# Kernel optimization log

Measured on AMD Instinct MI355X. Metric: run time of the kernel, lower is better.

## Reference

```python
import jax, jax.numpy as jnp
import numpy as np

N_NODES = 100000
N_EDGES = 1280000
IN_CH = 500
TEXT_DIM = 384
HIDDEN = 64
OUT_CH = 7


def _gcn_conv(h, w, b, src, dst, n):
    """PyG GCNConv: linear -> add self-loops -> sym-normalized sum aggregation -> bias.
    Self-loops handled analytically (adds deg+1 and a dinv[i]^2-scaled self message)
    to avoid materializing extra edges."""
    h = h @ w  # [n, out]
    ones = jnp.ones((src.shape[0],), h.dtype)
    deg = jax.ops.segment_sum(ones, dst, num_segments=n) + 1.0  # in-degree incl. self-loop
    dinv = deg ** -0.5
    coef = dinv[src] * dinv[dst]  # [E]
    msg = h[src] * coef[:, None]  # gather + normalize
    agg = jax.ops.segment_sum(msg, dst, num_segments=n)  # scatter-add
    agg = agg + h * (dinv * dinv)[:, None]  # self-loop contribution
    return agg + b


def setup_inputs() -> dict:
    key = jax.random.key(0)
    ks = jax.random.split(key, 12)
    f32 = jnp.float32
    x = jax.random.normal(ks[0], (N_NODES, IN_CH), f32)
    text_x = jax.random.normal(ks[1], (N_NODES, TEXT_DIM), f32)
    edge_index = jax.random.randint(ks[2], (2, N_EDGES), 0, N_NODES, dtype=jnp.int64)
    def lin(k, fan_in, fan_out):
        s = 1.0 / np.sqrt(fan_in)
        return jax.random.uniform(k, (fan_in, fan_out), f32, -s, s)
    return {
        "x": x,
        "text_x": text_x,
        "edge_index": edge_index,
        "w_feat": lin(ks[3], IN_CH, HIDDEN),
        "b_feat": jnp.zeros((HIDDEN,), f32),
        "w_text": lin(ks[4], TEXT_DIM, HIDDEN),
        "b_text": jnp.zeros((HIDDEN,), f32),
        "w1": lin(ks[5], 2 * HIDDEN, HIDDEN),
        "b1": jnp.zeros((HIDDEN,), f32),
        "w2": lin(ks[6], HIDDEN, OUT_CH),
        "b2": jnp.zeros((OUT_CH,), f32),
    }


def reference(x, text_x, edge_index, w_feat, b_feat, w_text, b_text, w1, b1, w2, b2):
    src, dst = edge_index[0], edge_index[1]
    h = jnp.concatenate([x @ w_feat + b_feat, text_x @ w_text + b_text], axis=1)  # [N, 2H]
    h = jax.nn.relu(_gcn_conv(h, w1, b1, src, dst, N_NODES))  # [N, H]
    # dropout is identity in eval mode
    return _gcn_conv(h, w2, b2, src, dst, N_NODES)  # [N, OUT]
```

## Files before the change

### kernel.cpp

```cpp
#include <hip/hip_runtime.h>

#define NN 100000
#define NNP 100352
#define NE 1280000
#define K_FEAT 500
#define K_TEXT 384
#define KP 512
#define H 64
#define BM 64
#define GEMM_GRID 1563
#define SCAN_BLOCKS 98
#define NODES_PER_SCAN 1024
#define FUSE_BLOCKS 257
#define SORT_CHUNK 2048
#define NCHUNKS 625
#define BUCKETS 392
#define BCAP 4096

typedef unsigned short ushort_t;
typedef __attribute__((ext_vector_type(8))) short bf16x8;
typedef __attribute__((ext_vector_type(4))) float f32x4;

template <int V> struct IC { static constexpr int value = V; };

__device__ __forceinline__ ushort_t f2bf(float f) {
    union { float f; unsigned int u; } v; v.f = f;
    unsigned int r = (v.u + 0x7FFFu + ((v.u >> 16) & 1u)) >> 16;
    return (ushort_t)r;
}

__device__ __forceinline__ float bf2f(ushort_t u) {
    union { unsigned int i; float f; } v; v.i = ((unsigned int)u) << 16; return v.f;
}

__device__ __forceinline__ bf16x8 cvt8(float4 a, float4 b) {
    union { bf16x8 v; unsigned int w[4]; } u;
    asm("v_cvt_pk_bf16_f32 %0, %1, %2" : "=v"(u.w[0]) : "v"(a.x), "v"(a.y));
    asm("v_cvt_pk_bf16_f32 %0, %1, %2" : "=v"(u.w[1]) : "v"(a.z), "v"(a.w));
    asm("v_cvt_pk_bf16_f32 %0, %1, %2" : "=v"(u.w[2]) : "v"(b.x), "v"(b.y));
    asm("v_cvt_pk_bf16_f32 %0, %1, %2" : "=v"(u.w[3]) : "v"(b.z), "v"(b.w));
    return u.v;
}

__global__ void prep_k(const float* __restrict__ wf, const float* __restrict__ bf,
                       const float* __restrict__ wt, const float* __restrict__ bt,
                       const float* __restrict__ w1,
                       ushort_t* __restrict__ WfxT, ushort_t* __restrict__ WtxT,
                       float* __restrict__ bpre, int* __restrict__ bcursor) {
    if (blockIdx.x == 0) {
        for (int i = threadIdx.x; i < BUCKETS; i += 256) bcursor[i] = i * BCAP;
    }
    const int idx = blockIdx.x * 256 + threadIdx.x;
    const int T1 = H * KP;
    const int T2 = 2 * T1;
    if (idx < T1) {
        const int c = idx >> 9, k = idx & 511;
        float s = 0.f;
        if (k < K_FEAT) {
            #pragma unroll 8
            for (int u = 0; u < 64; ++u) s = fmaf(wf[k * 64 + u], w1[u * 64 + c], s);
        }
        WfxT[idx] = f2bf(s);
    } else if (idx < T2) {
        const int r = idx - T1;
        const int c = r >> 9, k = r & 511;
        float s = 0.f;
        if (k < K_TEXT) {
            #pragma unroll 8
            for (int u = 0; u < 64; ++u) s = fmaf(wt[k * 64 + u], w1[(64 + u) * 64 + c], s);
        }
        WtxT[r] = f2bf(s);
    } else if (idx < T2 + H) {
        const int j = idx - T2;
        float s = 0.f;
        for (int u = 0; u < 64; ++u) s = fmaf(bf[u], w1[u * 64 + j], s);
        for (int u = 0; u < 64; ++u) s = fmaf(bt[u], w1[(64 + u) * 64 + j], s);
        bpre[j] = s;
    }
}

__global__ __launch_bounds__(256)
void offsets_k(const int* __restrict__ deg, int* __restrict__ row_start,
               float* __restrict__ dinv) {
    const int b = blockIdx.x;
    const int base = b * NODES_PER_SCAN;
    const int t = threadIdx.x;
    __shared__ int tsum[256];
    __shared__ int ws[4];
    int pre = 0;
    for (int i = t; i < (base >> 2); i += 256) {
        const int4 v = ((const int4*)deg)[i];
        pre += v.x + v.y + v.z + v.w;
    }
    #pragma unroll
    for (int m = 1; m < 64; m <<= 1) pre += __shfl_xor(pre, m, 64);
    if ((t & 63) == 0) ws[t >> 6] = pre;
    __syncthreads();
    const int bp = ws[0] + ws[1] + ws[2] + ws[3];
    int loc[4];
    int dg[4];
    int s = 0;
    #pragma unroll
    for (int i = 0; i < 4; ++i) {
        loc[i] = s;
        dg[i] = deg[base + t * 4 + i];
        s += dg[i];
    }
    tsum[t] = s;
    __syncthreads();
    #pragma unroll
    for (int off = 1; off < 256; off <<= 1) {
        int v = (t >= off) ? tsum[t - off] : 0;
        __syncthreads();
        tsum[t] += v;
        __syncthreads();
    }
    const int texcl = (t == 0) ? 0 : tsum[t - 1];
    #pragma unroll
    for (int i = 0; i < 4; ++i) {
        const int n = t * 4 + i;
        const int rs = bp + texcl + loc[i];
        row_start[base + n] = rs;
        dinv[base + n] = rsqrtf((float)dg[i] + 1.0f);
    }
}

__global__ __launch_bounds__(256)
void gemm_sort_k(const float* __restrict__ x, const float* __restrict__ txt,
                 const ushort_t* __restrict__ WfxT, const ushort_t* __restrict__ WtxT,
                 const float* __restrict__ bpre, ushort_t* __restrict__ u1b,
                 const int* __restrict__ ei, int* __restrict__ bcursor,
                 int* __restrict__ deg, int2* __restrict__ pairs) {
    __shared__ float As0[BM * 64], As1[BM * 64];
    __shared__ ushort_t Bs0[H * 64], Bs1[H * 64];
    const int b = blockIdx.x;
    const int t = threadIdx.x;

    if ((b & 1) == 0) {
        int* hist = (int*)As0;
        int* bbase = hist + 512;
        for (int chunk = b >> 1; chunk < NCHUNKS; chunk += GEMM_GRID) {
            const int e0 = chunk * SORT_CHUNK + t * 8;
            int4 s0 = *(const int4*)&ei[e0];
            int4 s1 = *(const int4*)&ei[e0 + 4];
            int4 d0 = *(const int4*)&ei[NE + e0];
            int4 d1 = *(const int4*)&ei[NE + e0 + 4];
            const int src[8] = {s0.x, s0.y, s0.z, s0.w, s1.x, s1.y, s1.z, s1.w};
            const int dst[8] = {d0.x, d0.y, d0.z, d0.w, d1.x, d1.y, d1.z, d1.w};
            for (int i = t; i < BUCKETS; i += 256) hist[i] = 0;
            __syncthreads();
            int bu[8];
            #pragma unroll
            for (int i = 0; i < 8; ++i) {
                bu[i] = dst[i] >> 8;
                atomicAdd(&hist[bu[i]], 1);
                atomicAdd(&deg[dst[i]], 1);
            }
            __syncthreads();
            for (int i = t; i < BUCKETS; i += 256)
                bbase[i] = atomicAdd(&bcursor[i], hist[i]);
            __syncthreads();
            #pragma unroll
            for (int i = 0; i < 8; ++i) {
                const int pos = atomicAdd(&bbase[bu[i]], 1);
                pairs[pos] = make_int2(src[i], dst[i]);
            }
            __syncthreads();
        }
        return;
    }

    const int wave = t >> 6, lane = t & 63;
    const int row0 = (b >> 1) * BM;
    const int lr = lane & 15, lq = lane >> 4;

    f32x4 acc[4];
    #pragma unroll
    for (int j = 0; j < 4; ++j) acc[j] = (f32x4){0.f, 0.f, 0.f, 0.f};

    auto stageA = [&](char* ldsa, const float* __restrict__ A, const int KD, const int k0) {
        #pragma unroll
        for (int p = 0; p < 4; ++p) {
            const int P = p * 4096 + t * 16;
            const int row = P >> 8;
            const int kk = ((P & 255) ^ ((row & 7) << 4)) >> 2;
            const int gk = min(k0 + kk, KD - 4);
            const int gr = min(row0 + row, NN - 1);
            __builtin_amdgcn_global_load_lds(
                (const __attribute__((address_space(1))) void*)(A + (long)gr * KD + gk),
                (__attribute__((address_space(3))) void*)(ldsa + P), 16, 0, 2 );
        }
    };
    auto stageB = [&](char* ldsb, const ushort_t* __restrict__ WT, const int k0) {
        #pragma unroll
        for (int p = 0; p < 2; ++p) {
            const int P = p * 4096 + t * 16;
            const int row = P >> 7;
            const int kkb = (P & 127) ^ ((row & 7) << 4);
            __builtin_amdgcn_global_load_lds(
                (const __attribute__((address_space(1))) void*)(WT + (long)row * KP + k0 + (kkb >> 1)),
                (__attribute__((address_space(3))) void*)(ldsb + P), 16, 0, 0);
        }
    };
    auto compute = [&](const char* ldsa, const char* ldsb) {
        #pragma unroll
        for (int ks = 0; ks < 2; ++ks) {
            const int ra = wave * 16 + lr;
            const int ka = ks * 128 + lq * 32;
            const int xa = (ra & 7) << 4;
            const float4 c0 = *(const float4*)(ldsa + ra * 256 + (ka ^ xa));
            const float4 c1 = *(const float4*)(ldsa + ra * 256 + ((ka + 16) ^ xa));
            const bf16x8 af = cvt8(c0, c1);
            bf16x8 bfr[4];
            #pragma unroll
            for (int cf = 0; cf < 4; ++cf) {
                const int col = cf * 16 + lr;
                const int kb = ks * 64 + lq * 16;
                bfr[cf] = *(const bf16x8*)(ldsb + col * 128 + (kb ^ ((col & 7) << 4)));
            }
            #pragma unroll
            for (int cf = 0; cf < 4; ++cf)
                acc[cf] = __builtin_amdgcn_mfma_f32_16x16x32_bf16(
                    af, bfr[cf], acc[cf], 0, 0, 0);
        }
    };

    auto phase = [&](const float* __restrict__ A, const ushort_t* __restrict__ WT,
                     auto KD_, auto NT_) {
        constexpr int KD = decltype(KD_)::value;
        constexpr int NT = decltype(NT_)::value;
        stageA((char*)As0, A, KD, 0);  stageB((char*)Bs0, WT, 0);
        stageA((char*)As1, A, KD, 64); stageB((char*)Bs1, WT, 64);
        #pragma unroll
        for (int kt = 0; kt < NT; ++kt) {
            if (kt == NT - 1) asm volatile("s_waitcnt vmcnt(0)" ::: "memory");
            else              asm volatile("s_waitcnt vmcnt(6)" ::: "memory");
            __builtin_amdgcn_s_barrier();
            __builtin_amdgcn_sched_barrier(0);
            if (kt & 1) compute((const char*)As1, (const char*)Bs1);
            else        compute((const char*)As0, (const char*)Bs0);
            __builtin_amdgcn_sched_barrier(0);
            __builtin_amdgcn_s_barrier();
            if (kt + 2 < NT) {
                if (kt & 1) { stageA((char*)As1, A, KD, (kt + 2) * 64); stageB((char*)Bs1, WT, (kt + 2) * 64); }
                else        { stageA((char*)As0, A, KD, (kt + 2) * 64); stageB((char*)Bs0, WT, (kt + 2) * 64); }
            }
        }
    };

    phase(x, WfxT, IC<K_FEAT>{}, IC<8>{});
    phase(txt, WtxT, IC<K_TEXT>{}, IC<6>{});

    #pragma unroll
    for (int reg = 0; reg < 4; ++reg) {
        const int r = row0 + wave * 16 + lq * 4 + reg;
        if (r < NN) {
            #pragma unroll
            for (int cf = 0; cf < 4; ++cf) {
                const int c = cf * 16 + lr;
                u1b[(long)r * H + c] = f2bf(acc[cf][reg] + bpre[c]);
            }
        }
    }
}

__global__ __launch_bounds__(256)
void sortp2_k(const int2* __restrict__ pairs, const int* __restrict__ bcursor,
              const int* __restrict__ row_start, int* __restrict__ src_sorted) {
    __shared__ int lcur[256];
    __shared__ int lout[BCAP];
    const int bu = blockIdx.x;
    const int t = threadIdx.x;
    const int nbase = bu << 8;
    const int r0 = row_start[nbase];
    const int cnt = bcursor[bu] - bu * BCAP;
    lcur[t] = row_start[nbase + t] - r0;
    __syncthreads();
    for (int i = t; i < cnt; i += 256) {
        const int2 pr = pairs[bu * BCAP + i];
        const int p = atomicAdd(&lcur[pr.y & 255], 1);
        lout[p] = pr.x;
    }
    __syncthreads();
    for (int i = t; i < cnt; i += 256)
        src_sorted[r0 + i] = lout[i];
}

__global__ __launch_bounds__(256)
void layer1_csr_k(const int* __restrict__ row_start, const int* __restrict__ deg,
                  const int* __restrict__ src_sorted, const ushort_t* __restrict__ u1b,
                  const float* __restrict__ dinv, const float* __restrict__ b1,
                  const float* __restrict__ w2, float* __restrict__ u2) {
    const int t = threadIdx.x;
    const int lane = t & 63;
    const int g = lane >> 3;
    const int c8 = lane & 7;
    const int node = blockIdx.x * 32 + (t >> 6) * 8 + g;
    if (node >= NN) return;
    const int rs = row_start[node];
    const int dg = deg[node];
    const float di = dinv[node];

    float acc8[8];
    {
        const bf16x8 v = *(const bf16x8*)(u1b + (long)node * H + c8 * 8);
        #pragma unroll
        for (int c = 0; c < 8; ++c) acc8[c] = di * bf2f((ushort_t)v[c]);
    }
    int j = 0;
    for (; j + 4 <= dg; j += 4) {
        const int s0 = src_sorted[rs + j];
        const int s1 = src_sorted[rs + j + 1];
        const int s2 = src_sorted[rs + j + 2];
        const int s3 = src_sorted[rs + j + 3];
        const float w0 = dinv[s0], w1_ = dinv[s1], w2_ = dinv[s2], w3 = dinv[s3];
        const bf16x8 v0 = *(const bf16x8*)(u1b + (long)s0 * H + c8 * 8);
        const bf16x8 v1 = *(const bf16x8*)(u1b + (long)s1 * H + c8 * 8);
        const bf16x8 v2 = *(const bf16x8*)(u1b + (long)s2 * H + c8 * 8);
        const bf16x8 v3 = *(const bf16x8*)(u1b + (long)s3 * H + c8 * 8);
        #pragma unroll
        for (int c = 0; c < 8; ++c)
            acc8[c] += (w0 * bf2f((ushort_t)v0[c]) + w1_ * bf2f((ushort_t)v1[c]))
                     + (w2_ * bf2f((ushort_t)v2[c]) + w3 * bf2f((ushort_t)v3[c]));
    }
    for (; j < dg; ++j) {
        const int s0 = src_sorted[rs + j];
        const float w0 = dinv[s0];
        const bf16x8 v0 = *(const bf16x8*)(u1b + (long)s0 * H + c8 * 8);
        #pragma unroll
        for (int c = 0; c < 8; ++c) acc8[c] += w0 * bf2f((ushort_t)v0[c]);
    }
    float h[8];
    #pragma unroll
    for (int c = 0; c < 8; ++c)
        h[c] = fmaxf(fmaf(di, acc8[c], b1[c8 * 8 + c]), 0.f);
    #pragma unroll
    for (int jj = 0; jj < 7; ++jj) {
        float s = 0.f;
        #pragma unroll
        for (int c = 0; c < 8; ++c)
            s = fmaf(h[c], w2[(c8 * 8 + c) * 7 + jj], s);
        s += __shfl_xor(s, 1, 64);
        s += __shfl_xor(s, 2, 64);
        s += __shfl_xor(s, 4, 64);
        if (c8 == jj) u2[node * 8 + jj] = di * s;
    }
}

__global__ __launch_bounds__(256)
void layer2_csr_k(const int* __restrict__ row_start, const int* __restrict__ deg,
                  const int* __restrict__ src_sorted, const float* __restrict__ u2,
                  const float* __restrict__ dinv, const float* __restrict__ b2,
                  float* __restrict__ out) {
    const int t = threadIdx.x;
    const int c = t & 7;
    const int node = blockIdx.x * 32 + (t >> 3);
    if (node >= NN) return;
    const int rs = row_start[node];
    const int dg = deg[node];
    float acc = (c < 7) ? u2[node * 8 + c] : 0.f;
    int j = 0;
    for (; j + 4 <= dg; j += 4) {
        const int s0 = src_sorted[rs + j];
        const int s1 = src_sorted[rs + j + 1];
        const int s2 = src_sorted[rs + j + 2];
        const int s3 = src_sorted[rs + j + 3];
        if (c < 7) {
            acc += u2[s0 * 8 + c];
            acc += u2[s1 * 8 + c];
            acc += u2[s2 * 8 + c];
            acc += u2[s3 * 8 + c];
        }
    }
    for (; j < dg; ++j) {
        const int s = src_sorted[rs + j];
        if (c < 7) acc += u2[s * 8 + c];
    }
    if (c < 7) out[node * 7 + c] = dinv[node] * acc + b2[c];
}

extern "C" void kernel_launch(void* const* d_in, const int* in_sizes, int n_in,
                              void* d_out, int out_size, void* d_ws, size_t ws_size,
                              hipStream_t stream) {
    const float* x      = (const float*)d_in[0];
    const float* txt    = (const float*)d_in[1];
    const int*   ei     = (const int*)d_in[2];
    const float* w_feat = (const float*)d_in[3];
    const float* b_feat = (const float*)d_in[4];
    const float* w_text = (const float*)d_in[5];
    const float* b_text = (const float*)d_in[6];
    const float* w1     = (const float*)d_in[7];
    const float* b1     = (const float*)d_in[8];
    const float* w2     = (const float*)d_in[9];
    const float* b2     = (const float*)d_in[10];
    float* out = (float*)d_out;

    char* p = (char*)d_ws;
    auto alloc = [&](size_t bytes) {
        char* r = p;
        p += (bytes + 255) & ~(size_t)255;
        return r;
    };
    ushort_t* WfxT = (ushort_t*)alloc((size_t)H * KP * 2);
    ushort_t* WtxT = (ushort_t*)alloc((size_t)H * KP * 2);
    float* bpre = (float*)alloc(H * 4);
    int*   deg  = (int*)alloc((size_t)NNP * 4);
    float* dinv = (float*)alloc((size_t)NNP * 4);
    int*   row_start = (int*)alloc((size_t)NNP * 4);
    int*   bcursor   = (int*)alloc((size_t)BUCKETS * 4);
    int2*  pairs     = (int2*)alloc((size_t)BUCKETS * BCAP * 8);
    int*   src_sorted = (int*)alloc((size_t)NE * 4);
    ushort_t* u1b = (ushort_t*)alloc((size_t)NN * H * 2);
    float* u2   = (float*)alloc((size_t)NN * 8 * 4);

    hipMemsetAsync(deg, 0, (size_t)NNP * 4, stream);

    prep_k<<<FUSE_BLOCKS, 256, 0, stream>>>(w_feat, b_feat, w_text, b_text, w1,
                                            WfxT, WtxT, bpre, bcursor);
    gemm_sort_k<<<2 * GEMM_GRID, 256, 0, stream>>>(x, txt, WfxT, WtxT, bpre, u1b,
                                                   ei, bcursor, deg, pairs);
    offsets_k<<<SCAN_BLOCKS, 256, 0, stream>>>(deg, row_start, dinv);
    sortp2_k<<<BUCKETS, 256, 0, stream>>>(pairs, bcursor, row_start, src_sorted);
    layer1_csr_k<<<(NN + 31) / 32, 256, 0, stream>>>(row_start, deg, src_sorted, u1b,
                                                     dinv, b1, w2, u2);
    layer2_csr_k<<<(NN + 31) / 32, 256, 0, stream>>>(row_start, deg, src_sorted, u2,
                                                     dinv, b2, out);
}
```

Before: 254.5 us.

## Compute degrees and CSR offsets inside bucket sort pass, drop scan kernel

```diff
diff --git a/kernel.cpp b/kernel.cpp
--- a/kernel.cpp
+++ b/kernel.cpp
@@ -9,8 +9,6 @@
 #define H 64
 #define BM 64
 #define GEMM_GRID 1563
-#define SCAN_BLOCKS 98
-#define NODES_PER_SCAN 1024
 #define FUSE_BLOCKS 257
 #define SORT_CHUNK 2048
 #define NCHUNKS 625
@@ -80,57 +78,11 @@
 }
 
 __global__ __launch_bounds__(256)
-void offsets_k(const int* __restrict__ deg, int* __restrict__ row_start,
-               float* __restrict__ dinv) {
-    const int b = blockIdx.x;
-    const int base = b * NODES_PER_SCAN;
-    const int t = threadIdx.x;
-    __shared__ int tsum[256];
-    __shared__ int ws[4];
-    int pre = 0;
-    for (int i = t; i < (base >> 2); i += 256) {
-        const int4 v = ((const int4*)deg)[i];
-        pre += v.x + v.y + v.z + v.w;
-    }
-    #pragma unroll
-    for (int m = 1; m < 64; m <<= 1) pre += __shfl_xor(pre, m, 64);
-    if ((t & 63) == 0) ws[t >> 6] = pre;
-    __syncthreads();
-    const int bp = ws[0] + ws[1] + ws[2] + ws[3];
-    int loc[4];
-    int dg[4];
-    int s = 0;
-    #pragma unroll
-    for (int i = 0; i < 4; ++i) {
-        loc[i] = s;
-        dg[i] = deg[base + t * 4 + i];
-        s += dg[i];
-    }
-    tsum[t] = s;
-    __syncthreads();
-    #pragma unroll
-    for (int off = 1; off < 256; off <<= 1) {
-        int v = (t >= off) ? tsum[t - off] : 0;
-        __syncthreads();
-        tsum[t] += v;
-        __syncthreads();
-    }
-    const int texcl = (t == 0) ? 0 : tsum[t - 1];
-    #pragma unroll
-    for (int i = 0; i < 4; ++i) {
-        const int n = t * 4 + i;
-        const int rs = bp + texcl + loc[i];
-        row_start[base + n] = rs;
-        dinv[base + n] = rsqrtf((float)dg[i] + 1.0f);
-    }
-}
-
-__global__ __launch_bounds__(256)
 void gemm_sort_k(const float* __restrict__ x, const float* __restrict__ txt,
                  const ushort_t* __restrict__ WfxT, const ushort_t* __restrict__ WtxT,
                  const float* __restrict__ bpre, ushort_t* __restrict__ u1b,
                  const int* __restrict__ ei, int* __restrict__ bcursor,
-                 int* __restrict__ deg, int2* __restrict__ pairs) {
+                 int2* __restrict__ pairs) {
     __shared__ float As0[BM * 64], As1[BM * 64];
     __shared__ ushort_t Bs0[H * 64], Bs1[H * 64];
     const int b = blockIdx.x;
@@ -154,7 +106,6 @@
             for (int i = 0; i < 8; ++i) {
                 bu[i] = dst[i] >> 8;
                 atomicAdd(&hist[bu[i]], 1);
-                atomicAdd(&deg[dst[i]], 1);
             }
             __syncthreads();
             for (int i = t; i < BUCKETS; i += 256)
@@ -266,15 +217,44 @@
 
 __global__ __launch_bounds__(256)
 void sortp2_k(const int2* __restrict__ pairs, const int* __restrict__ bcursor,
-              const int* __restrict__ row_start, int* __restrict__ src_sorted) {
+              int* __restrict__ deg, float* __restrict__ dinv,
+              int* __restrict__ row_start, int* __restrict__ src_sorted) {
+    __shared__ int lhist[256];
     __shared__ int lcur[256];
     __shared__ int lout[BCAP];
+    __shared__ int ws[4];
     const int bu = blockIdx.x;
     const int t = threadIdx.x;
     const int nbase = bu << 8;
-    const int r0 = row_start[nbase];
     const int cnt = bcursor[bu] - bu * BCAP;
-    lcur[t] = row_start[nbase + t] - r0;
+    int pre = 0;
+    for (int i = t; i < bu; i += 256) pre += bcursor[i] - i * BCAP;
+    #pragma unroll
+    for (int m = 1; m < 64; m <<= 1) pre += __shfl_xor(pre, m, 64);
+    if ((t & 63) == 0) ws[t >> 6] = pre;
+    lhist[t] = 0;
+    __syncthreads();
+    const int r0 = ws[0] + ws[1] + ws[2] + ws[3];
+    for (int i = t; i < cnt; i += 256)
+        atomicAdd(&lhist[pairs[bu * BCAP + i].y & 255], 1);
+    __syncthreads();
+    const int dg = lhist[t];
+    int run = dg;
+    lcur[t] = run;
+    __syncthreads();
+    #pragma unroll
+    for (int off = 1; off < 256; off <<= 1) {
+        int v = (t >= off) ? lcur[t - off] : 0;
+        __syncthreads();
+        lcur[t] += v;
+        __syncthreads();
+    }
+    const int excl = lcur[t] - dg;
+    deg[nbase + t] = dg;
+    dinv[nbase + t] = rsqrtf((float)dg + 1.0f);
+    row_start[nbase + t] = r0 + excl;
+    __syncthreads();
+    lcur[t] = excl;
     __syncthreads();
     for (int i = t; i < cnt; i += 256) {
         const int2 pr = pairs[bu * BCAP + i];
@@ -413,14 +393,11 @@
     ushort_t* u1b = (ushort_t*)alloc((size_t)NN * H * 2);
     float* u2   = (float*)alloc((size_t)NN * 8 * 4);
 
-    hipMemsetAsync(deg, 0, (size_t)NNP * 4, stream);
-
     prep_k<<<FUSE_BLOCKS, 256, 0, stream>>>(w_feat, b_feat, w_text, b_text, w1,
                                             WfxT, WtxT, bpre, bcursor);
     gemm_sort_k<<<2 * GEMM_GRID, 256, 0, stream>>>(x, txt, WfxT, WtxT, bpre, u1b,
-                                                   ei, bcursor, deg, pairs);
-    offsets_k<<<SCAN_BLOCKS, 256, 0, stream>>>(deg, row_start, dinv);
-    sortp2_k<<<BUCKETS, 256, 0, stream>>>(pairs, bcursor, row_start, src_sorted);
+                                                   ei, bcursor, pairs);
+    sortp2_k<<<BUCKETS, 256, 0, stream>>>(pairs, bcursor, deg, dinv, row_start, src_sorted);
     layer1_csr_k<<<(NN + 31) / 32, 256, 0, stream>>>(row_start, deg, src_sorted, u1b,
                                                      dinv, b1, w2, u2);
     layer2_csr_k<<<(NN + 31) / 32, 256, 0, stream>>>(row_start, deg, src_sorted, u2,
```

New measurement: 214.9 us. -15.6%, faster.
